# Kernel tuning notes

Hardware: AMD Instinct MI355X
Metric: run time of the kernel (lower is better)

The kernel has to match this reference:

```python
import jax, jax.numpy as jnp
import numpy as np

D_MODEL = 1024
NUM_HEADS = 16
D_K = D_MODEL // NUM_HEADS


def setup_inputs() -> dict:
    key = jax.random.key(0)
    ks = jax.random.split(key, 9)
    s = 1.0 / np.sqrt(D_MODEL)
    x = jax.random.normal(ks[0], (2, 2048, D_MODEL), dtype=jnp.float32)
    Wq = jax.random.uniform(ks[1], (D_MODEL, D_MODEL), jnp.float32, -s, s)
    bq = jax.random.uniform(ks[2], (D_MODEL,), jnp.float32, -s, s)
    Wk = jax.random.uniform(ks[3], (D_MODEL, D_MODEL), jnp.float32, -s, s)
    bk = jax.random.uniform(ks[4], (D_MODEL,), jnp.float32, -s, s)
    Wv = jax.random.uniform(ks[5], (D_MODEL, D_MODEL), jnp.float32, -s, s)
    bv = jax.random.uniform(ks[6], (D_MODEL,), jnp.float32, -s, s)
    Wo = jax.random.uniform(ks[7], (D_MODEL, D_MODEL), jnp.float32, -s, s)
    bo = jax.random.uniform(ks[8], (D_MODEL,), jnp.float32, -s, s)
    return {"x": x, "Wq": Wq, "bq": bq, "Wk": Wk, "bk": bk,
            "Wv": Wv, "bv": bv, "Wo": Wo, "bo": bo}


def reference(x, Wq, bq, Wk, bk, Wv, bv, Wo, bo):
    B, S, _ = x.shape
    # torch Linear: y = x @ W.T + b
    def proj(W, b):
        h = x @ W.T + b                       # [B,S,D]
        return h.reshape(B, S, NUM_HEADS, D_K).transpose(0, 2, 1, 3)  # [B,H,S,Dk]
    Q = proj(Wq, bq)
    K = proj(Wk, bk)
    V = proj(Wv, bv)
    scale = 1.0 / np.sqrt(D_K)
    scores = jnp.einsum('bhqd,bhkd->bhqk', Q, K) * scale   # [B,H,S,S]
    causal = jnp.triu(jnp.ones((S, S), dtype=bool), k=1)   # True above diag
    scores = jnp.where(causal, -jnp.inf, scores)
    probs = jax.nn.softmax(scores, axis=-1)
    out = jnp.einsum('bhqk,bhkd->bhqd', probs, V)          # [B,H,S,Dk]
    out = out.transpose(0, 2, 1, 3).reshape(B, S, NUM_HEADS * D_K)
    return out @ Wo.T + bo
```

## Files before the change

### kernel.cpp

```cpp
#include <hip/hip_runtime.h>

typedef unsigned short u16;
typedef __attribute__((ext_vector_type(8))) short short8;
typedef __attribute__((ext_vector_type(4))) float floatx4;

__device__ __forceinline__ u16 f2bf(float x){
  union { float f; unsigned u; } v; v.f = x;
  unsigned r = v.u + 0x7fffu + ((v.u >> 16) & 1u);
  return (u16)(r >> 16);
}

__device__ __forceinline__ unsigned cvt_pk_bf16(float lo, float hi){
  unsigned r;
  asm("v_cvt_pk_bf16_f32 %0, %1, %2" : "=v"(r) : "v"(lo), "v"(hi));
  return r;
}

__device__ __forceinline__ void gld16(const u16* g, u16* l){
  __builtin_amdgcn_global_load_lds(
      (const __attribute__((address_space(1))) void*)g,
      (__attribute__((address_space(3))) void*)l, 16, 0, 0);
}

__global__ void k_cvt_all(const float* __restrict__ x,
                          const float* __restrict__ wq, const float* __restrict__ wk,
                          const float* __restrict__ wv, const float* __restrict__ wo,
                          u16* __restrict__ xb, u16* __restrict__ wqb, u16* __restrict__ wkb,
                          u16* __restrict__ wvb, u16* __restrict__ wob){
  const int i = blockIdx.x * 256 + threadIdx.x;
  const float* s; u16* d; int off;
  if (i < 1048576) { s = x; d = xb; off = i; }
  else {
    const int j = i - 1048576;
    const int wsel = j >> 18;
    off = j & 262143;
    s = (wsel==0) ? wq : (wsel==1) ? wk : (wsel==2) ? wv : wo;
    d = (wsel==0) ? wqb : (wsel==1) ? wkb : (wsel==2) ? wvb : wob;
  }
  const float4 f = ((const float4*)s)[off];
  unsigned lo = (unsigned)f2bf(f.x) | ((unsigned)f2bf(f.y) << 16);
  unsigned hi = (unsigned)f2bf(f.z) | ((unsigned)f2bf(f.w) << 16);
  ((uint2*)d)[off] = make_uint2(lo, hi);
}

__global__ __launch_bounds__(256) void k_gemm_qkv(
    const u16* __restrict__ A,
    const u16* __restrict__ Wq, const u16* __restrict__ Wk, const u16* __restrict__ Wv,
    const float* __restrict__ bq, const float* __restrict__ bk, const float* __restrict__ bv,
    u16* __restrict__ Qo, u16* __restrict__ Ko, u16* __restrict__ Vo)
{
  const int bid = (int)blockIdx.x;
  const int xcd = bid & 7;
  const int i5  = bid >> 3;
  const int xb_ = ((xcd >> 2) << 2) + (i5 & 3);
  const int rest = i5 >> 2;
  const int yb_ = ((xcd & 3) << 3) + (rest & 7);
  const int mode = rest >> 3;

  const u16* W      = (mode==1) ? Wk : (mode==2) ? Wv : Wq;
  const float* bias = (mode==1) ? bk : (mode==2) ? bv : bq;

  __shared__ u16 lA[2][4096];
  __shared__ u16 lB[2][4096];

  const int tid  = threadIdx.x;
  const int row0 = yb_ * 128;
  const int col0 = xb_ * 128;

  const int srow = tid >> 2;
  const int sgp  = tid & 3;
  const int sgl  = sgp ^ ((srow >> 1) & 3);
  const u16* ga0 = A + (row0 + srow)      * 1024 + sgl * 8;
  const u16* ga1 = A + (row0 + srow + 64) * 1024 + sgl * 8;
  const u16* gb0 = W + (col0 + srow)      * 1024 + sgl * 8;
  const u16* gb1 = W + (col0 + srow + 64) * 1024 + sgl * 8;

  const int l  = tid & 63, w = tid >> 6;
  const int wr = w >> 1,  wc = w & 1;
  const int lr = l & 15,  grp = l >> 4;
  const int sw = (lr >> 1) & 3;
  int aoff[4], boff[4];
#pragma unroll
  for (int m = 0; m < 4; ++m) aoff[m] = (wr*64 + m*16 + lr)*32 + ((grp ^ sw) * 8);
#pragma unroll
  for (int n = 0; n < 4; ++n) boff[n] = (wc*64 + n*16 + lr)*32 + ((grp ^ sw) * 8);

  floatx4 acc[4][4];
#pragma unroll
  for (int m = 0; m < 4; ++m)
#pragma unroll
    for (int n = 0; n < 4; ++n) acc[m][n] = (floatx4){0.f, 0.f, 0.f, 0.f};

#define STAGE(buf, kt_) do { \
    const int k0_ = (kt_) * 32; \
    gld16(ga0 + k0_, &lA[(buf)][tid*8]); \
    gld16(ga1 + k0_, &lA[(buf)][2048 + tid*8]); \
    gld16(gb0 + k0_, &lB[(buf)][tid*8]); \
    gld16(gb1 + k0_, &lB[(buf)][2048 + tid*8]); \
  } while (0)

  STAGE(0, 0);
  __syncthreads();
  for (int kt = 0; kt < 32; ++kt) {
    const int cur = kt & 1;
    if (kt < 31) STAGE(cur ^ 1, kt + 1);
    short8 af[4], bf[4];
#pragma unroll
    for (int m = 0; m < 4; ++m) af[m] = *(const short8*)&lA[cur][aoff[m]];
#pragma unroll
    for (int n = 0; n < 4; ++n) bf[n] = *(const short8*)&lB[cur][boff[n]];
#pragma unroll
    for (int m = 0; m < 4; ++m)
#pragma unroll
      for (int n = 0; n < 4; ++n)
        acc[m][n] = __builtin_amdgcn_mfma_f32_16x16x32_bf16(af[m], bf[n], acc[m][n], 0, 0, 0);
    __syncthreads();
  }
#undef STAGE

  const float sc = (mode == 0) ? 0.18033688011112042f : 1.0f;
  u16* dst = (mode == 0) ? Qo : (mode == 1) ? Ko : Vo;
#pragma unroll
  for (int n = 0; n < 4; ++n) {
    const int cg = col0 + wc*64 + n*16 + lr;
    const float bb = bias[cg];
    const int h = cg >> 6, d = cg & 63;
#pragma unroll
    for (int m = 0; m < 4; ++m) {
#pragma unroll
      for (int j = 0; j < 4; ++j) {
        const int rg = row0 + wr*64 + m*16 + grp*4 + j;
        const int b = rg >> 11, s5 = rg & 2047;
        const float val = (acc[m][n][j] + bb) * sc;
        int idx;
        if (mode == 2) idx = ((b*16 + h)*64 + d)*2048 + s5;
        else           idx = ((b*16 + h)*2048 + s5)*64 + d;
        dst[idx] = f2bf(val);
      }
    }
  }
}

__global__ __launch_bounds__(256) void k_gemm_o(
    const u16* __restrict__ A, const u16* __restrict__ W,
    const float* __restrict__ bias, float* __restrict__ Fo)
{
  const int bid = (int)blockIdx.x;
  const int xcd = bid & 7;
  const int i5  = bid >> 3;
  const int xb_ = ((xcd >> 2) << 2) + (i5 & 3);
  const int yb_ = ((xcd & 3) << 4) + (i5 >> 2);

  __shared__ u16 lA[2][2048];
  __shared__ u16 lB[2][4096];

  const int tid  = threadIdx.x;
  const int row0 = yb_ * 64;
  const int col0 = xb_ * 128;

  const int srow = tid >> 2;
  const int sgp  = tid & 3;
  const int sgl  = sgp ^ ((srow >> 1) & 3);
  const u16* ga0 = A + (row0 + srow)      * 1024 + sgl * 8;
  const u16* gb0 = W + (col0 + srow)      * 1024 + sgl * 8;
  const u16* gb1 = W + (col0 + srow + 64) * 1024 + sgl * 8;

  const int l  = tid & 63, w = tid >> 6;
  const int wr = w >> 1,  wc = w & 1;
  const int lr = l & 15,  grp = l >> 4;
  const int sw = (lr >> 1) & 3;
  int aoff[2], boff[4];
#pragma unroll
  for (int m = 0; m < 2; ++m) aoff[m] = (wr*32 + m*16 + lr)*32 + ((grp ^ sw) * 8);
#pragma unroll
  for (int n = 0; n < 4; ++n) boff[n] = (wc*64 + n*16 + lr)*32 + ((grp ^ sw) * 8);

  floatx4 acc[2][4];
#pragma unroll
  for (int m = 0; m < 2; ++m)
#pragma unroll
    for (int n = 0; n < 4; ++n) acc[m][n] = (floatx4){0.f, 0.f, 0.f, 0.f};

#define STAGE(buf, kt_) do { \
    const int k0_ = (kt_) * 32; \
    gld16(ga0 + k0_, &lA[(buf)][tid*8]); \
    gld16(gb0 + k0_, &lB[(buf)][tid*8]); \
    gld16(gb1 + k0_, &lB[(buf)][2048 + tid*8]); \
  } while (0)

  STAGE(0, 0);
  __syncthreads();
  for (int kt = 0; kt < 32; ++kt) {
    const int cur = kt & 1;
    if (kt < 31) STAGE(cur ^ 1, kt + 1);
    short8 af[2], bf[4];
#pragma unroll
    for (int m = 0; m < 2; ++m) af[m] = *(const short8*)&lA[cur][aoff[m]];
#pragma unroll
    for (int n = 0; n < 4; ++n) bf[n] = *(const short8*)&lB[cur][boff[n]];
#pragma unroll
    for (int m = 0; m < 2; ++m)
#pragma unroll
      for (int n = 0; n < 4; ++n)
        acc[m][n] = __builtin_amdgcn_mfma_f32_16x16x32_bf16(af[m], bf[n], acc[m][n], 0, 0, 0);
    __syncthreads();
  }
#undef STAGE

#pragma unroll
  for (int n = 0; n < 4; ++n) {
    const int cg = col0 + wc*64 + n*16 + lr;
    const float bb = bias[cg];
#pragma unroll
    for (int m = 0; m < 2; ++m) {
      const int rg = row0 + wr*32 + m*16 + grp*4;
#pragma unroll
      for (int j = 0; j < 4; ++j)
        Fo[(rg + j) * 1024 + cg] = acc[m][n][j] + bb;
    }
  }
}

__global__ __launch_bounds__(256, 2) void k_attn(
    const u16* __restrict__ Q, const u16* __restrict__ K,
    const u16* __restrict__ V, u16* __restrict__ O)
{
  __shared__ u16 lK[4][4096];
  __shared__ u16 lV[4][4096];
  __shared__ u16 lP[4][1024];

  const int tid = threadIdx.x;
  const int bid = (int)blockIdx.x;
  const int xcd = bid & 7, r = bid >> 3;
  const int bh = xcd * 4 + (r >> 4);
  const int pr = r & 15;

  const int l = tid & 63, w = tid >> 6;
  const int lr = l & 15, grp = l >> 4;

  const u16* Qh = Q + (size_t)bh * 2048 * 64;
  const u16* Kh = K + (size_t)bh * 2048 * 64;
  const u16* Vh = V + (size_t)bh * 64 * 2048;

  const int srow = tid >> 3, sgp = tid & 7;
  const int sgl = sgp ^ (srow & 7);
  u16* lPw = &lP[w][0];
  const int swz = lr & 7;
  const int b = bh >> 4, h = bh & 15;

#define STAGEKV(buf, kt_) do { \
    gld16(Kh + ((kt_)*64 + srow     )*64 + sgl*8, &lK[(buf)][tid*8]); \
    gld16(Kh + ((kt_)*64 + srow + 32)*64 + sgl*8, &lK[(buf)][2048 + tid*8]); \
    gld16(Vh + (srow     )*2048 + (kt_)*64 + sgl*8, &lV[(buf)][tid*8]); \
    gld16(Vh + (srow + 32)*2048 + (kt_)*64 + sgl*8, &lV[(buf)][2048 + tid*8]); \
  } while (0)

#pragma unroll
  for (int pass = 0; pass < 2; ++pass) {
    const int qt = pass ? pr : (31 - pr);
    const int qw0 = qt * 64 + w * 16;
    const int nkt = qt + 1;

    short8 qf[2];
#pragma unroll
    for (int kk = 0; kk < 2; ++kk)
      qf[kk] = *(const short8*)(Qh + (qw0 + lr)*64 + kk*32 + grp*8);

    floatx4 accO[4];
    float mrow = -1e30f, lrow = 0.f;
#pragma unroll
    for (int dn = 0; dn < 4; ++dn) accO[dn] = (floatx4){0.f, 0.f, 0.f, 0.f};

    STAGEKV(0, 0);
    if (nkt > 1) STAGEKV(1, 1);
    __syncthreads();

    for (int kt2 = 0; kt2 < nkt; kt2 += 2) {
      if (kt2 + 2 < nkt) STAGEKV((kt2 + 2) & 3, kt2 + 2);
      if (kt2 + 3 < nkt) STAGEKV((kt2 + 3) & 3, kt2 + 3);

#pragma unroll
      for (int half = 0; half < 2; ++half) {
        const int kt = kt2 + half;
        if (half == 1 && kt >= nkt) break;
        const int cur = kt & 3;
        const int kb = kt * 64;

        floatx4 st[4];
#pragma unroll
        for (int n = 0; n < 4; ++n) st[n] = (floatx4){0.f, 0.f, 0.f, 0.f};
#pragma unroll
        for (int n = 0; n < 4; ++n) {
          const int key = n*16 + lr;
#pragma unroll
          for (int kk = 0; kk < 2; ++kk) {
            const int gp = (kk*4 + grp) ^ (key & 7);
            short8 kf = *(const short8*)&lK[cur][key*64 + gp*8];
            st[n] = __builtin_amdgcn_mfma_f32_16x16x32_bf16(kf, qf[kk], st[n], 0, 0, 0);
          }
        }

        const int lim = qw0 + lr - kb;
        if (63 > lim) {
#pragma unroll
          for (int n = 0; n < 4; ++n)
#pragma unroll
            for (int j = 0; j < 4; ++j)
              if (n*16 + grp*4 + j > lim) st[n][j] = -1e30f;
        }

        float mt = st[0][0];
#pragma unroll
        for (int n = 0; n < 4; ++n)
#pragma unroll
          for (int j = 0; j < 4; ++j) mt = fmaxf(mt, st[n][j]);
        if (!__all(mt <= mrow)) {
          float mg = fmaxf(mt, __shfl_xor(mt, 16));
          mg = fmaxf(mg, __shfl_xor(mg, 32));
          const float mn = fmaxf(mrow, mg);
          const float alpha = exp2f(mrow - mn);
          mrow = mn;
          lrow *= alpha;
#pragma unroll
          for (int dn = 0; dn < 4; ++dn) accO[dn] *= alpha;
        }
        float ps = 0.f;
#pragma unroll
        for (int n = 0; n < 4; ++n)
#pragma unroll
          for (int j = 0; j < 4; ++j) {
            const float p = exp2f(st[n][j] - mrow);
            st[n][j] = p;
            ps += p;
          }
        lrow += ps;

#pragma unroll
        for (int n = 0; n < 4; ++n)
#pragma unroll
          for (int p2 = 0; p2 < 2; ++p2) {
            const unsigned pk = cvt_pk_bf16(st[n][2*p2], st[n][2*p2+1]);
            const int pg = (2*n + (grp >> 1)) ^ swz;
            ((unsigned*)lPw)[lr*32 + pg*4 + (grp & 1)*2 + p2] = pk;
          }

        asm volatile("s_waitcnt lgkmcnt(0)" ::: "memory");

        short8 pa[2];
#pragma unroll
        for (int kk = 0; kk < 2; ++kk)
          pa[kk] = *(const short8*)&lPw[lr*64 + (((kk*4 + grp) ^ swz) * 8)];

#pragma unroll
        for (int dn = 0; dn < 4; ++dn) {
          const int d = dn*16 + lr;
#pragma unroll
          for (int kk = 0; kk < 2; ++kk) {
            const int gp = (kk*4 + grp) ^ (d & 7);
            short8 vf = *(const short8*)&lV[cur][d*64 + gp*8];
            accO[dn] = __builtin_amdgcn_mfma_f32_16x16x32_bf16(vf, pa[kk], accO[dn], 0, 0, 0);
          }
        }
      }
      __syncthreads();
    }

    float lt = lrow + __shfl_xor(lrow, 16);
    lt += __shfl_xor(lt, 32);
    const float inv = 1.0f / lt;
    const int token = b*2048 + qw0 + lr;
#pragma unroll
    for (int dn = 0; dn < 4; ++dn)
#pragma unroll
      for (int p2 = 0; p2 < 2; ++p2) {
        const unsigned pk = cvt_pk_bf16(accO[dn][2*p2] * inv, accO[dn][2*p2+1] * inv);
        *(unsigned*)&O[token*1024 + h*64 + dn*16 + grp*4 + 2*p2] = pk;
      }
  }
#undef STAGEKV
}

extern "C" void kernel_launch(void* const* d_in, const int* in_sizes, int n_in,
                              void* d_out, int out_size, void* d_ws, size_t ws_size,
                              hipStream_t stream) {
  const float* x  = (const float*)d_in[0];
  const float* Wq = (const float*)d_in[1];
  const float* bq = (const float*)d_in[2];
  const float* Wk = (const float*)d_in[3];
  const float* bk = (const float*)d_in[4];
  const float* Wv = (const float*)d_in[5];
  const float* bv = (const float*)d_in[6];
  const float* Wo = (const float*)d_in[7];
  const float* bo = (const float*)d_in[8];
  float* out = (float*)d_out;

  char* ws = (char*)d_ws;
  u16* xb  = (u16*)(ws + 0);
  u16* wqb = (u16*)(ws + 8388608);
  u16* wkb = (u16*)(ws + 10485760);
  u16* wvb = (u16*)(ws + 12582912);
  u16* wob = (u16*)(ws + 14680064);
  u16* Qb  = (u16*)(ws + 16777216);
  u16* Kb  = (u16*)(ws + 25165824);
  u16* Vb  = (u16*)(ws + 33554432);
  u16* Ab  = (u16*)(ws + 41943040);

  k_cvt_all<<<dim3(8192), 256, 0, stream>>>(x, Wq, Wk, Wv, Wo, xb, wqb, wkb, wvb, wob);

  k_gemm_qkv<<<dim3(768), 256, 0, stream>>>(xb, wqb, wkb, wvb, bq, bk, bv, Qb, Kb, Vb);

  k_attn<<<dim3(512), 256, 0, stream>>>(Qb, Kb, Vb, Ab);

  k_gemm_o<<<dim3(512), 256, 0, stream>>>(Ab, wob, bo, out);
}
```

Before: 123.3 us.

## Use three-stage LDS pipelines with partial vmcnt waits in GEMMs and attention

Both projection GEMMs move from double to triple buffering in LDS. They prefetch two k-tiles ahead and replace __syncthreads with an s_waitcnt on a partial vmcnt count plus s_barrier, so the next tile's global loads can stay in flight across the barrier. The attention kernel trades its four-buffer, two-tile-per-barrier scheme for three buffers with one barrier per tile and the same partial-wait barrier. This lowers LDS use in attention but adds barriers there, and it depends on exact hand-coded vmcnt counts matching the number of outstanding loads.

```diff
diff --git a/kernel.cpp b/kernel.cpp
--- a/kernel.cpp
+++ b/kernel.cpp
@@ -21,6 +21,10 @@
       (const __attribute__((address_space(1))) void*)g,
       (__attribute__((address_space(3))) void*)l, 16, 0, 0);
 }
+
+#define WAIT_BAR_V4() asm volatile("s_waitcnt vmcnt(4) lgkmcnt(0)\ns_barrier" ::: "memory")
+#define WAIT_BAR_V3() asm volatile("s_waitcnt vmcnt(3) lgkmcnt(0)\ns_barrier" ::: "memory")
+#define WAIT_BAR_V0() asm volatile("s_waitcnt vmcnt(0) lgkmcnt(0)\ns_barrier" ::: "memory")
 
 __global__ void k_cvt_all(const float* __restrict__ x,
                           const float* __restrict__ wq, const float* __restrict__ wk,
@@ -60,8 +64,8 @@
   const u16* W      = (mode==1) ? Wk : (mode==2) ? Wv : Wq;
   const float* bias = (mode==1) ? bk : (mode==2) ? bv : bq;
 
-  __shared__ u16 lA[2][4096];
-  __shared__ u16 lB[2][4096];
+  __shared__ u16 lA[3][4096];
+  __shared__ u16 lB[3][4096];
 
   const int tid  = threadIdx.x;
   const int row0 = yb_ * 128;
@@ -100,10 +104,13 @@
   } while (0)
 
   STAGE(0, 0);
-  __syncthreads();
+  STAGE(1, 1);
+  asm volatile("s_waitcnt vmcnt(4)\ns_barrier" ::: "memory");
+
   for (int kt = 0; kt < 32; ++kt) {
-    const int cur = kt & 1;
-    if (kt < 31) STAGE(cur ^ 1, kt + 1);
+    const int cur = kt % 3;
+    const bool st2 = (kt + 2 < 32);
+    if (st2) STAGE((kt + 2) % 3, kt + 2);
     short8 af[4], bf[4];
 #pragma unroll
     for (int m = 0; m < 4; ++m) af[m] = *(const short8*)&lA[cur][aoff[m]];
@@ -114,7 +121,7 @@
 #pragma unroll
       for (int n = 0; n < 4; ++n)
         acc[m][n] = __builtin_amdgcn_mfma_f32_16x16x32_bf16(af[m], bf[n], acc[m][n], 0, 0, 0);
-    __syncthreads();
+    if (st2) WAIT_BAR_V4(); else WAIT_BAR_V0();
   }
 #undef STAGE
 
@@ -151,8 +158,8 @@
   const int xb_ = ((xcd >> 2) << 2) + (i5 & 3);
   const int yb_ = ((xcd & 3) << 4) + (i5 >> 2);
 
-  __shared__ u16 lA[2][2048];
-  __shared__ u16 lB[2][4096];
+  __shared__ u16 lA[3][2048];
+  __shared__ u16 lB[3][4096];
 
   const int tid  = threadIdx.x;
   const int row0 = yb_ * 64;
@@ -189,10 +196,13 @@
   } while (0)
 
   STAGE(0, 0);
-  __syncthreads();
+  STAGE(1, 1);
+  asm volatile("s_waitcnt vmcnt(3)\ns_barrier" ::: "memory");
+
   for (int kt = 0; kt < 32; ++kt) {
-    const int cur = kt & 1;
-    if (kt < 31) STAGE(cur ^ 1, kt + 1);
+    const int cur = kt % 3;
+    const bool st2 = (kt + 2 < 32);
+    if (st2) STAGE((kt + 2) % 3, kt + 2);
     short8 af[2], bf[4];
 #pragma unroll
     for (int m = 0; m < 2; ++m) af[m] = *(const short8*)&lA[cur][aoff[m]];
@@ -203,7 +213,7 @@
 #pragma unroll
       for (int n = 0; n < 4; ++n)
         acc[m][n] = __builtin_amdgcn_mfma_f32_16x16x32_bf16(af[m], bf[n], acc[m][n], 0, 0, 0);
-    __syncthreads();
+    if (st2) WAIT_BAR_V3(); else WAIT_BAR_V0();
   }
 #undef STAGE
 
@@ -225,8 +235,8 @@
     const u16* __restrict__ Q, const u16* __restrict__ K,
     const u16* __restrict__ V, u16* __restrict__ O)
 {
-  __shared__ u16 lK[4][4096];
-  __shared__ u16 lV[4][4096];
+  __shared__ u16 lK[3][4096];
+  __shared__ u16 lV[3][4096];
   __shared__ u16 lP[4][1024];
 
   const int tid = threadIdx.x;
@@ -272,97 +282,96 @@
     for (int dn = 0; dn < 4; ++dn) accO[dn] = (floatx4){0.f, 0.f, 0.f, 0.f};
 
     STAGEKV(0, 0);
-    if (nkt > 1) STAGEKV(1, 1);
-    __syncthreads();
-
-    for (int kt2 = 0; kt2 < nkt; kt2 += 2) {
-      if (kt2 + 2 < nkt) STAGEKV((kt2 + 2) & 3, kt2 + 2);
-      if (kt2 + 3 < nkt) STAGEKV((kt2 + 3) & 3, kt2 + 3);
-
-#pragma unroll
-      for (int half = 0; half < 2; ++half) {
-        const int kt = kt2 + half;
-        if (half == 1 && kt >= nkt) break;
-        const int cur = kt & 3;
-        const int kb = kt * 64;
-
-        floatx4 st[4];
-#pragma unroll
-        for (int n = 0; n < 4; ++n) st[n] = (floatx4){0.f, 0.f, 0.f, 0.f};
-#pragma unroll
-        for (int n = 0; n < 4; ++n) {
-          const int key = n*16 + lr;
-#pragma unroll
-          for (int kk = 0; kk < 2; ++kk) {
-            const int gp = (kk*4 + grp) ^ (key & 7);
-            short8 kf = *(const short8*)&lK[cur][key*64 + gp*8];
-            st[n] = __builtin_amdgcn_mfma_f32_16x16x32_bf16(kf, qf[kk], st[n], 0, 0, 0);
-          }
+    if (nkt > 1) {
+      STAGEKV(1, 1);
+      asm volatile("s_waitcnt vmcnt(4)\ns_barrier" ::: "memory");
+    } else {
+      asm volatile("s_waitcnt vmcnt(0)\ns_barrier" ::: "memory");
+    }
+
+    for (int kt = 0; kt < nkt; ++kt) {
+      const int cur = kt % 3;
+      const bool st2 = (kt + 2 < nkt);
+      if (st2) STAGEKV((kt + 2) % 3, kt + 2);
+      const int kb = kt * 64;
+
+      floatx4 st[4];
+#pragma unroll
+      for (int n = 0; n < 4; ++n) st[n] = (floatx4){0.f, 0.f, 0.f, 0.f};
+#pragma unroll
+      for (int n = 0; n < 4; ++n) {
+        const int key = n*16 + lr;
+#pragma unroll
+        for (int kk = 0; kk < 2; ++kk) {
+          const int gp = (kk*4 + grp) ^ (key & 7);
+          short8 kf = *(const short8*)&lK[cur][key*64 + gp*8];
+          st[n] = __builtin_amdgcn_mfma_f32_16x16x32_bf16(kf, qf[kk], st[n], 0, 0, 0);
         }
-
-        const int lim = qw0 + lr - kb;
-        if (63 > lim) {
-#pragma unroll
-          for (int n = 0; n < 4; ++n)
-#pragma unroll
-            for (int j = 0; j < 4; ++j)
-              if (n*16 + grp*4 + j > lim) st[n][j] = -1e30f;
+      }
+
+      const int lim = qw0 + lr - kb;
+      if (63 > lim) {
+#pragma unroll
+        for (int n = 0; n < 4; ++n)
+#pragma unroll
+          for (int j = 0; j < 4; ++j)
+            if (n*16 + grp*4 + j > lim) st[n][j] = -1e30f;
+      }
+
+      float mt = st[0][0];
+#pragma unroll
+      for (int n = 0; n < 4; ++n)
+#pragma unroll
+        for (int j = 0; j < 4; ++j) mt = fmaxf(mt, st[n][j]);
+      if (!__all(mt <= mrow)) {
+        float mg = fmaxf(mt, __shfl_xor(mt, 16));
+        mg = fmaxf(mg, __shfl_xor(mg, 32));
+        const float mn = fmaxf(mrow, mg);
+        const float alpha = exp2f(mrow - mn);
+        mrow = mn;
+        lrow *= alpha;
+#pragma unroll
+        for (int dn = 0; dn < 4; ++dn) accO[dn] *= alpha;
+      }
+      float ps = 0.f;
+#pragma unroll
+      for (int n = 0; n < 4; ++n)
+#pragma unroll
+        for (int j = 0; j < 4; ++j) {
+          const float p = exp2f(st[n][j] - mrow);
+          st[n][j] = p;
+          ps += p;
         }
-
-        float mt = st[0][0];
-#pragma unroll
-        for (int n = 0; n < 4; ++n)
-#pragma unroll
-          for (int j = 0; j < 4; ++j) mt = fmaxf(mt, st[n][j]);
-        if (!__all(mt <= mrow)) {
-          float mg = fmaxf(mt, __shfl_xor(mt, 16));
-          mg = fmaxf(mg, __shfl_xor(mg, 32));
-          const float mn = fmaxf(mrow, mg);
-          const float alpha = exp2f(mrow - mn);
-          mrow = mn;
-          lrow *= alpha;
-#pragma unroll
-          for (int dn = 0; dn < 4; ++dn) accO[dn] *= alpha;
+      lrow += ps;
+
+#pragma unroll
+      for (int n = 0; n < 4; ++n)
+#pragma unroll
+        for (int p2 = 0; p2 < 2; ++p2) {
+          const unsigned pk = cvt_pk_bf16(st[n][2*p2], st[n][2*p2+1]);
+          const int pg = (2*n + (grp >> 1)) ^ swz;
+          ((unsigned*)lPw)[lr*32 + pg*4 + (grp & 1)*2 + p2] = pk;
         }
-        float ps = 0.f;
-#pragma unroll
-        for (int n = 0; n < 4; ++n)
-#pragma unroll
-          for (int j = 0; j < 4; ++j) {
-            const float p = exp2f(st[n][j] - mrow);
-            st[n][j] = p;
-            ps += p;
-          }
-        lrow += ps;
-
-#pragma unroll
-        for (int n = 0; n < 4; ++n)
-#pragma unroll
-          for (int p2 = 0; p2 < 2; ++p2) {
-            const unsigned pk = cvt_pk_bf16(st[n][2*p2], st[n][2*p2+1]);
-            const int pg = (2*n + (grp >> 1)) ^ swz;
-            ((unsigned*)lPw)[lr*32 + pg*4 + (grp & 1)*2 + p2] = pk;
-          }
-
-        asm volatile("s_waitcnt lgkmcnt(0)" ::: "memory");
-
-        short8 pa[2];
-#pragma unroll
-        for (int kk = 0; kk < 2; ++kk)
-          pa[kk] = *(const short8*)&lPw[lr*64 + (((kk*4 + grp) ^ swz) * 8)];
-
-#pragma unroll
-        for (int dn = 0; dn < 4; ++dn) {
-          const int d = dn*16 + lr;
-#pragma unroll
-          for (int kk = 0; kk < 2; ++kk) {
-            const int gp = (kk*4 + grp) ^ (d & 7);
-            short8 vf = *(const short8*)&lV[cur][d*64 + gp*8];
-            accO[dn] = __builtin_amdgcn_mfma_f32_16x16x32_bf16(vf, pa[kk], accO[dn], 0, 0, 0);
-          }
+
+      asm volatile("s_waitcnt lgkmcnt(0)" ::: "memory");
+
+      short8 pa[2];
+#pragma unroll
+      for (int kk = 0; kk < 2; ++kk)
+        pa[kk] = *(const short8*)&lPw[lr*64 + (((kk*4 + grp) ^ swz) * 8)];
+
+#pragma unroll
+      for (int dn = 0; dn < 4; ++dn) {
+        const int d = dn*16 + lr;
+#pragma unroll
+        for (int kk = 0; kk < 2; ++kk) {
+          const int gp = (kk*4 + grp) ^ (d & 7);
+          short8 vf = *(const short8*)&lV[cur][d*64 + gp*8];
+          accO[dn] = __builtin_amdgcn_mfma_f32_16x16x32_bf16(vf, pa[kk], accO[dn], 0, 0, 0);
         }
       }
-      __syncthreads();
+
+      if (st2) WAIT_BAR_V4(); else WAIT_BAR_V0();
     }
 
     float lt = lrow + __shfl_xor(lrow, 16);
```

New measurement: 121.6 us. About the same (-1.4%).
